# Performance work log

Hardware: AMD Instinct MI355X
Metric: run time of the kernel (lower is better)

The kernel has to match this reference:

```python
import jax, jax.numpy as jnp
import numpy as np


def setup_inputs() -> dict:
    key = jax.random.key(0)
    ks = jax.random.split(key, 5)
    B, DEC, ENC, H = 4, 256, 256, 512  # feature_dim = hl_size = 512, mlp hidden = 512
    decoder_states = jax.random.normal(ks[0], (B, DEC, H), dtype=jnp.float32)
    encoder_states = jax.random.normal(ks[1], (B, ENC, H), dtype=jnp.float32)
    ext_mask = jnp.zeros((B, DEC, ENC), dtype=bool)  # self.mask set externally; all-False here
    W_mlp = jax.random.normal(ks[2], (2 * H, H), dtype=jnp.float32) * 0.02  # Linear(2H -> H)
    b_mlp = jnp.zeros((H,), dtype=jnp.float32)
    W_out = jax.random.normal(ks[3], (H, 1), dtype=jnp.float32) * 0.02  # Linear(H -> 1)
    b_out = jnp.zeros((1,), dtype=jnp.float32)
    return {"decoder_states": decoder_states, "encoder_states": encoder_states,
            "ext_mask": ext_mask, "W_mlp": W_mlp, "b_mlp": b_mlp,
            "W_out": W_out, "b_out": b_out}


def reference(decoder_states, encoder_states, ext_mask, W_mlp, b_mlp, W_out, b_out):
    # decoder_states: [B, dec, H]; encoder_states: [B, enc, H]
    H = encoder_states.shape[-1]
    # pad mask: positions where encoder feature-0 equals 0.0 -> [B, 1, enc]
    pad_mask = (encoder_states == 0.0)[:, :, :1]
    pad_mask = jnp.swapaxes(pad_mask, 1, 2)  # [B, 1, enc]
    # cat(enc, dec) @ W_mlp  ==  enc @ W_mlp[:H] + dec @ W_mlp[H:]  (avoids 2H concat)
    enc_proj = jnp.einsum('beh,hm->bem', encoder_states, W_mlp[:H])   # [B, enc, Hm]
    dec_proj = jnp.einsum('bdh,hm->bdm', decoder_states, W_mlp[H:])   # [B, dec, Hm]
    hidden = jnp.tanh(dec_proj[:, :, None, :] + enc_proj[:, None, :, :] + b_mlp)  # [B, dec, enc, Hm]
    attn = jnp.einsum('bdem,mo->bde', hidden, W_out) + b_out[0]       # [B, dec, enc]
    attn = jnp.where(ext_mask, -jnp.inf, attn)
    attn = jnp.where(pad_mask, -jnp.inf, attn)
    attn = jax.nn.softmax(attn, axis=-1)
    context = jnp.einsum('bde,beh->bdh', attn, encoder_states)        # [B, dec, H]
    return (context, attn)
```

## Files before the change

### kernel.cpp

```cpp
#include <hip/hip_runtime.h>
#include <math.h>

#define B 4
#define DEC 256
#define ENC 256
#define HDIM 512

#define TANH_SCALE 2.8853900817779268f
#define LOG2E 1.4426950408889634f

__device__ __forceinline__ float fast_exp2(float x) { return __builtin_amdgcn_exp2f(x); }
__device__ __forceinline__ float fast_rcp(float x)  { return __builtin_amdgcn_rcpf(x); }

typedef __attribute__((ext_vector_type(8))) short bf16x8;
typedef __attribute__((ext_vector_type(4))) short bf16x4;
typedef __attribute__((ext_vector_type(4))) float f32x4;

__device__ __forceinline__ unsigned short bf16_rne(float x) {
    unsigned u = __float_as_uint(x);
    return (unsigned short)((u + 0x7FFFu + ((u >> 16) & 1u)) >> 16);
}
__device__ __forceinline__ float bf16_to_f(unsigned short h) {
    return __uint_as_float((unsigned)h << 16);
}

#define W_OFS(m, k) ((((long)(m) >> 4) << 13) + (((long)(k) >> 3) << 7) + (((m) & 15) << 3) + ((k) & 7))

__global__ __launch_bounds__(256) void convert_kernel(
    const float* __restrict__ enc, const float* __restrict__ dec,
    const float* __restrict__ Wmlp,
    unsigned short* __restrict__ Xh_e, unsigned short* __restrict__ Xl_e,
    unsigned short* __restrict__ Xh_d, unsigned short* __restrict__ Xl_d,
    unsigned short* __restrict__ Wh_e, unsigned short* __restrict__ Wl_e,
    unsigned short* __restrict__ Wh_d, unsigned short* __restrict__ Wl_d)
{
    const int tid = threadIdx.x, z = blockIdx.z;
    if (z < 2) {
        const float* X = z ? dec : enc;
        unsigned short* H = z ? Xh_d : Xh_e;
        unsigned short* L = z ? Xl_d : Xl_e;
        const long i8 = ((long)blockIdx.x * 256 + tid) * 8;
        float4 v0 = *(const float4*)(X + i8);
        float4 v1 = *(const float4*)(X + i8 + 4);
        float xs[8] = {v0.x, v0.y, v0.z, v0.w, v1.x, v1.y, v1.z, v1.w};
        bf16x8 hv, lv;
#pragma unroll
        for (int j = 0; j < 8; ++j) {
            unsigned short h = bf16_rne(xs[j]);
            hv[j] = (short)h;
            lv[j] = (short)bf16_rne(xs[j] - bf16_to_f(h));
        }
        *(bf16x8*)(H + i8) = hv;
        *(bf16x8*)(L + i8) = lv;
    } else {
        const float* Wsrc = Wmlp + (z == 3 ? (long)HDIM * HDIM : 0);
        unsigned short* H = (z == 3) ? Wh_d : Wh_e;
        unsigned short* L = (z == 3) ? Wl_d : Wl_e;
        const int t = blockIdx.x * 256 + tid;
        const int m = t & 511;
        const int k0 = (t >> 9) << 2;
        bf16x4 hv, lv;
#pragma unroll
        for (int j = 0; j < 4; ++j) {
            float x = Wsrc[(long)(k0 + j) * 512 + m];
            unsigned short h = bf16_rne(x);
            hv[j] = (short)h;
            lv[j] = (short)bf16_rne(x - bf16_to_f(h));
        }
        const long ofs = W_OFS(m, k0);
        *(bf16x4*)(H + ofs) = hv;
        *(bf16x4*)(L + ofs) = lv;
    }
}

__global__ __launch_bounds__(256) void proj_mfma_kernel(
    const unsigned short* __restrict__ Xh_e, const unsigned short* __restrict__ Xl_e,
    const unsigned short* __restrict__ Xh_d, const unsigned short* __restrict__ Xl_d,
    const unsigned short* __restrict__ Wh_e, const unsigned short* __restrict__ Wl_e,
    const unsigned short* __restrict__ Wh_d, const unsigned short* __restrict__ Wl_d,
    const float* __restrict__ bmlp,
    float* __restrict__ ET, float* __restrict__ Dmat)
{
    const int tid = threadIdx.x;
    const int wave = tid >> 6, lane = tid & 63;
    const int z = blockIdx.z;
    const int r0w = blockIdx.x * 64 + wave * 16;
    const int m0 = blockIdx.y * 32;
    const unsigned short* Xh = z ? Xh_d : Xh_e;
    const unsigned short* Xl = z ? Xl_d : Xl_e;
    const unsigned short* Wh = z ? Wh_d : Wh_e;
    const unsigned short* Wl = z ? Wl_d : Wl_e;

    const int col = lane & 15;
    const int quad = lane >> 4;

    const unsigned short* pah = Xh + (long)(r0w + col) * 512 + quad * 8;
    const unsigned short* pal = Xl + (long)(r0w + col) * 512 + quad * 8;
    const long bofs = ((long)(m0 >> 4) << 13) + (quad << 7) + (col << 3);
    const unsigned short* pb0h = Wh + bofs;
    const unsigned short* pb0l = Wl + bofs;
    const unsigned short* pb1h = Wh + bofs + 8192;
    const unsigned short* pb1l = Wl + bofs + 8192;

    f32x4 a0h = {0.f,0.f,0.f,0.f}, a0x = {0.f,0.f,0.f,0.f};
    f32x4 a1h = {0.f,0.f,0.f,0.f}, a1x = {0.f,0.f,0.f,0.f};

    bf16x8 Ah = *(const bf16x8*)pah,  Al = *(const bf16x8*)pal;
    bf16x8 B0h = *(const bf16x8*)pb0h, B0l = *(const bf16x8*)pb0l;
    bf16x8 B1h = *(const bf16x8*)pb1h, B1l = *(const bf16x8*)pb1l;

#pragma unroll 1
    for (int k0 = 0; k0 < 512; k0 += 32) {
        bf16x8 nAh = Ah, nAl = Al, nB0h = B0h, nB0l = B0l, nB1h = B1h, nB1l = B1l;
        if (k0 + 32 < 512) {
            nAh = *(const bf16x8*)(pah + k0 + 32);
            nAl = *(const bf16x8*)(pal + k0 + 32);
            const long ko = (long)(k0 + 32) << 4;
            nB0h = *(const bf16x8*)(pb0h + ko);
            nB0l = *(const bf16x8*)(pb0l + ko);
            nB1h = *(const bf16x8*)(pb1h + ko);
            nB1l = *(const bf16x8*)(pb1l + ko);
        }
        a0h = __builtin_amdgcn_mfma_f32_16x16x32_bf16(Ah, B0h, a0h, 0, 0, 0);
        a1h = __builtin_amdgcn_mfma_f32_16x16x32_bf16(Ah, B1h, a1h, 0, 0, 0);
        a0x = __builtin_amdgcn_mfma_f32_16x16x32_bf16(Ah, B0l, a0x, 0, 0, 0);
        a1x = __builtin_amdgcn_mfma_f32_16x16x32_bf16(Ah, B1l, a1x, 0, 0, 0);
        a0x = __builtin_amdgcn_mfma_f32_16x16x32_bf16(Al, B0h, a0x, 0, 0, 0);
        a1x = __builtin_amdgcn_mfma_f32_16x16x32_bf16(Al, B1h, a1x, 0, 0, 0);
        Ah = nAh; Al = nAl; B0h = nB0h; B0l = nB0l; B1h = nB1h; B1l = nB1l;
    }

    if (z == 0) {
        const int batch = r0w >> 8;
        const int e0 = (r0w & 255) + quad * 4;
        float* base = ET + (long)batch * HDIM * ENC;
        float4 v;
        v.x = fast_exp2((a0h[0] + a0x[0]) * TANH_SCALE);
        v.y = fast_exp2((a0h[1] + a0x[1]) * TANH_SCALE);
        v.z = fast_exp2((a0h[2] + a0x[2]) * TANH_SCALE);
        v.w = fast_exp2((a0h[3] + a0x[3]) * TANH_SCALE);
        *(float4*)&base[(long)(m0 + col) * ENC + e0] = v;
        v.x = fast_exp2((a1h[0] + a1x[0]) * TANH_SCALE);
        v.y = fast_exp2((a1h[1] + a1x[1]) * TANH_SCALE);
        v.z = fast_exp2((a1h[2] + a1x[2]) * TANH_SCALE);
        v.w = fast_exp2((a1h[3] + a1x[3]) * TANH_SCALE);
        *(float4*)&base[(long)(m0 + 16 + col) * ENC + e0] = v;
    } else {
        const float bq0 = bmlp[m0 + col];
        const float bq1 = bmlp[m0 + 16 + col];
        const int r = r0w + quad * 4;
#pragma unroll
        for (int i = 0; i < 4; ++i) {
            Dmat[(long)(r + i) * HDIM + m0 + col] =
                fast_exp2((a0h[i] + a0x[i] + bq0) * TANH_SCALE);
            Dmat[(long)(r + i) * HDIM + m0 + 16 + col] =
                fast_exp2((a1h[i] + a1x[i] + bq1) * TANH_SCALE);
        }
    }
}

__global__ __launch_bounds__(512) void attn_ctx_kernel(
    const float* __restrict__ Dmat, const float* __restrict__ ET,
    const float* __restrict__ wo,
    const float* __restrict__ enc, const unsigned char* __restrict__ extm,
    float* __restrict__ attn_out, float* __restrict__ ctx)
{
    __shared__ __align__(16) float ds[4][HDIM];
    __shared__ __align__(16) float wos[HDIM];
    __shared__ __align__(16) float p2[2][4][ENC];
    __shared__ __align__(16) float as4T[ENC][4];
    __shared__ float redm[4][4];
    __shared__ float reds[4][4];

    const int tid = threadIdx.x;
    const int b = blockIdx.z, d0 = blockIdx.x * 4;
    const long g0 = (long)b * DEC + d0;

    ((float4*)ds)[tid] = ((const float4*)(Dmat + g0 * HDIM))[tid];
    if (tid < 128) ((float4*)wos)[tid] = ((const float4*)wo)[tid];

    const int ty = tid >> 8;
    const int e = tid & 255;
    const float* ecol = ET + (long)b * HDIM * ENC + (long)(ty * 256) * ENC + e;

    float ev[16], nv[16];
#pragma unroll
    for (int j = 0; j < 16; ++j) ev[j] = ecol[j * ENC];
    __syncthreads();

    float acc[4] = {0.f, 0.f, 0.f, 0.f};
    for (int m = 0; m < 256; m += 16) {
        if (m + 16 < 256) {
#pragma unroll
            for (int j = 0; j < 16; ++j) nv[j] = ecol[(m + 16 + j) * ENC];
        }
        const int mb = ty * 256 + m;
        float4 dv[4][4], wv[4];
#pragma unroll
        for (int q = 0; q < 4; ++q) {
#pragma unroll
            for (int r = 0; r < 4; ++r)
                dv[r][q] = *(const float4*)&ds[r][mb + q * 4];
            wv[q] = *(const float4*)&wos[mb + q * 4];
        }
#pragma unroll
        for (int j = 0; j < 16; ++j) {
            float w = ((const float*)&wv[j >> 2])[j & 3];
#pragma unroll
            for (int r = 0; r < 4; ++r) {
                float t = fmaf(ev[j], ((const float*)&dv[r][j >> 2])[j & 3], 1.0f);
                acc[r] = fmaf(w, fast_rcp(t), acc[r]);
            }
        }
#pragma unroll
        for (int j = 0; j < 16; ++j) ev[j] = nv[j];
    }

#pragma unroll
    for (int r = 0; r < 4; ++r) p2[ty][r][e] = acc[r];
    __syncthreads();

    float l[4], p[4];
    const int wave = tid >> 6, lane = tid & 63;
    if (ty == 0) {
        const bool pad = (enc[((long)b * ENC + e) * HDIM] == 0.0f);
#pragma unroll
        for (int r = 0; r < 4; ++r) {
            float a = p2[0][r][e] + p2[1][r][e];
            bool xm = extm[(g0 + r) * ENC + e] != 0;
            l[r] = (pad || xm) ? -__builtin_inff() : -2.0f * a;
        }
        float mx[4] = {l[0], l[1], l[2], l[3]};
#pragma unroll
        for (int off = 32; off >= 1; off >>= 1) {
#pragma unroll
            for (int r = 0; r < 4; ++r)
                mx[r] = fmaxf(mx[r], __shfl_xor(mx[r], off, 64));
        }
        if (lane == 0) {
#pragma unroll
            for (int r = 0; r < 4; ++r) redm[wave][r] = mx[r];
        }
    }
    __syncthreads();
    if (ty == 0) {
        float s[4];
#pragma unroll
        for (int r = 0; r < 4; ++r) {
            float gm = fmaxf(fmaxf(redm[0][r], redm[1][r]),
                             fmaxf(redm[2][r], redm[3][r]));
            p[r] = fast_exp2((l[r] - gm) * LOG2E);
            s[r] = p[r];
        }
#pragma unroll
        for (int off = 32; off >= 1; off >>= 1) {
#pragma unroll
            for (int r = 0; r < 4; ++r)
                s[r] += __shfl_xor(s[r], off, 64);
        }
        if (lane == 0) {
#pragma unroll
            for (int r = 0; r < 4; ++r) reds[wave][r] = s[r];
        }
    }
    __syncthreads();
    if (ty == 0) {
        float4 pv;
        float pr[4];
#pragma unroll
        for (int r = 0; r < 4; ++r) {
            float gs = reds[0][r] + reds[1][r] + reds[2][r] + reds[3][r];
            pr[r] = p[r] * fast_rcp(gs);
            attn_out[(g0 + r) * ENC + e] = pr[r];
        }
        pv.x = pr[0]; pv.y = pr[1]; pv.z = pr[2]; pv.w = pr[3];
        *(float4*)&as4T[e][0] = pv;
    }
    __syncthreads();

    const int h = tid;
    const float* eh = enc + (long)b * ENC * HDIM + h;
    float ac0 = 0.f, ac1 = 0.f, ac2 = 0.f, ac3 = 0.f;
    float ebuf[8], nbuf[8];
#pragma unroll
    for (int j = 0; j < 8; ++j) ebuf[j] = eh[(long)j * HDIM];
    for (int e0 = 0; e0 < ENC; e0 += 8) {
        if (e0 + 8 < ENC) {
#pragma unroll
            for (int j = 0; j < 8; ++j) nbuf[j] = eh[(long)(e0 + 8 + j) * HDIM];
        }
#pragma unroll
        for (int j = 0; j < 8; ++j) {
            float4 prv = *(const float4*)&as4T[e0 + j][0];
            float ev4 = ebuf[j];
            ac0 = fmaf(prv.x, ev4, ac0);
            ac1 = fmaf(prv.y, ev4, ac1);
            ac2 = fmaf(prv.z, ev4, ac2);
            ac3 = fmaf(prv.w, ev4, ac3);
        }
#pragma unroll
        for (int j = 0; j < 8; ++j) ebuf[j] = nbuf[j];
    }
    ctx[(g0 + 0) * HDIM + h] = ac0;
    ctx[(g0 + 1) * HDIM + h] = ac1;
    ctx[(g0 + 2) * HDIM + h] = ac2;
    ctx[(g0 + 3) * HDIM + h] = ac3;
}

extern "C" void kernel_launch(void* const* d_in, const int* in_sizes, int n_in,
                              void* d_out, int out_size, void* d_ws, size_t ws_size,
                              hipStream_t stream) {
    const float* dec = (const float*)d_in[0];
    const float* enc = (const float*)d_in[1];
    const unsigned char* extm = (const unsigned char*)d_in[2];
    const float* Wmlp = (const float*)d_in[3];
    const float* bmlp = (const float*)d_in[4];
    const float* Wout = (const float*)d_in[5];

    float* ctx = (float*)d_out;
    float* attn = ctx + (size_t)B * DEC * HDIM;

    const size_t F = (size_t)B * DEC * HDIM;
    float* ET = (float*)d_ws;
    float* Dmat = ET + F;
    unsigned short* Xh_e = (unsigned short*)(Dmat + F);
    unsigned short* Xl_e = Xh_e + F;
    unsigned short* Xh_d = Xl_e + F;
    unsigned short* Xl_d = Xh_d + F;
    unsigned short* Wh_e = Xl_d + F;
    unsigned short* Wl_e = Wh_e + HDIM * HDIM;
    unsigned short* Wh_d = Wl_e + HDIM * HDIM;
    unsigned short* Wl_d = Wh_d + HDIM * HDIM;

    convert_kernel<<<dim3(256, 1, 4), 256, 0, stream>>>(
        enc, dec, Wmlp, Xh_e, Xl_e, Xh_d, Xl_d, Wh_e, Wl_e, Wh_d, Wl_d);
    proj_mfma_kernel<<<dim3(16, 16, 2), 256, 0, stream>>>(
        Xh_e, Xl_e, Xh_d, Xl_d, Wh_e, Wl_e, Wh_d, Wl_d, bmlp, ET, Dmat);
    attn_ctx_kernel<<<dim3(DEC / 4, 1, B), 512, 0, stream>>>(
        Dmat, ET, Wout, enc, extm, attn, ctx);
}
```

Measured before the change: 118.0 us.

## Retile attention score loop to 8 m-groups x 4 enc columns per thread

Each thread now covers 4 encoder columns (float4 loads) over a 64-wide slice of the hidden dim, in place of one column over 256 hidden values. The 8 partial sums are reduced through a larger shared buffer. The softmax stage is spread across all 512 threads, each handling 2 decoder rows, so half the block no longer sits idle. The aims are vectorized global loads, fewer LDS reads per reciprocal, and better thread use in the softmax. The cost is more shared memory for the partial sums and a longer reduction over 8 partials.

```diff
diff --git a/kernel.cpp b/kernel.cpp
--- a/kernel.cpp
+++ b/kernel.cpp
@@ -167,7 +167,7 @@
 {
     __shared__ __align__(16) float ds[4][HDIM];
     __shared__ __align__(16) float wos[HDIM];
-    __shared__ __align__(16) float p2[2][4][ENC];
+    __shared__ __align__(16) float p8[8][4][ENC];
     __shared__ __align__(16) float as4T[ENC][4];
     __shared__ float redm[4][4];
     __shared__ float reds[4][4];
@@ -179,102 +179,98 @@
     ((float4*)ds)[tid] = ((const float4*)(Dmat + g0 * HDIM))[tid];
     if (tid < 128) ((float4*)wos)[tid] = ((const float4*)wo)[tid];
 
+    const int mg = tid >> 6;
+    const int e4 = (tid & 63) * 4;
+    const int mbase = mg * 64;
+    const float* ep = ET + (long)b * HDIM * ENC + (long)mbase * ENC + e4;
+
+    float4 E0 = *(const float4*)(ep);
+    float4 E1 = *(const float4*)(ep + ENC);
+    __syncthreads();
+
+    float acc[4][4] = {};
+    for (int i = 0; i < 64; i += 2) {
+        float4 Ea = E0, Eb = E1;
+        if (i + 2 < 64) {
+            E0 = *(const float4*)(ep + (long)(i + 2) * ENC);
+            E1 = *(const float4*)(ep + (long)(i + 3) * ENC);
+        }
+        const int m = mbase + i;
+        const float w0 = wos[m], w1 = wos[m + 1];
+#pragma unroll
+        for (int r = 0; r < 4; ++r) {
+            const float dr0 = ds[r][m];
+            const float dr1 = ds[r][m + 1];
+#pragma unroll
+            for (int j = 0; j < 4; ++j) {
+                float ea = ((const float*)&Ea)[j];
+                float eb = ((const float*)&Eb)[j];
+                acc[r][j] = fmaf(w0, fast_rcp(fmaf(ea, dr0, 1.0f)), acc[r][j]);
+                acc[r][j] = fmaf(w1, fast_rcp(fmaf(eb, dr1, 1.0f)), acc[r][j]);
+            }
+        }
+    }
+#pragma unroll
+    for (int r = 0; r < 4; ++r) {
+        float4 v = make_float4(acc[r][0], acc[r][1], acc[r][2], acc[r][3]);
+        *(float4*)&p8[mg][r][e4] = v;
+    }
+    __syncthreads();
+
     const int ty = tid >> 8;
     const int e = tid & 255;
-    const float* ecol = ET + (long)b * HDIM * ENC + (long)(ty * 256) * ENC + e;
-
-    float ev[16], nv[16];
-#pragma unroll
-    for (int j = 0; j < 16; ++j) ev[j] = ecol[j * ENC];
-    __syncthreads();
-
-    float acc[4] = {0.f, 0.f, 0.f, 0.f};
-    for (int m = 0; m < 256; m += 16) {
-        if (m + 16 < 256) {
-#pragma unroll
-            for (int j = 0; j < 16; ++j) nv[j] = ecol[(m + 16 + j) * ENC];
-        }
-        const int mb = ty * 256 + m;
-        float4 dv[4][4], wv[4];
-#pragma unroll
-        for (int q = 0; q < 4; ++q) {
-#pragma unroll
-            for (int r = 0; r < 4; ++r)
-                dv[r][q] = *(const float4*)&ds[r][mb + q * 4];
-            wv[q] = *(const float4*)&wos[mb + q * 4];
-        }
-#pragma unroll
-        for (int j = 0; j < 16; ++j) {
-            float w = ((const float*)&wv[j >> 2])[j & 3];
-#pragma unroll
-            for (int r = 0; r < 4; ++r) {
-                float t = fmaf(ev[j], ((const float*)&dv[r][j >> 2])[j & 3], 1.0f);
-                acc[r] = fmaf(w, fast_rcp(t), acc[r]);
-            }
-        }
-#pragma unroll
-        for (int j = 0; j < 16; ++j) ev[j] = nv[j];
-    }
-
-#pragma unroll
-    for (int r = 0; r < 4; ++r) p2[ty][r][e] = acc[r];
-    __syncthreads();
-
-    float l[4], p[4];
     const int wave = tid >> 6, lane = tid & 63;
-    if (ty == 0) {
-        const bool pad = (enc[((long)b * ENC + e) * HDIM] == 0.0f);
-#pragma unroll
-        for (int r = 0; r < 4; ++r) {
-            float a = p2[0][r][e] + p2[1][r][e];
-            bool xm = extm[(g0 + r) * ENC + e] != 0;
-            l[r] = (pad || xm) ? -__builtin_inff() : -2.0f * a;
-        }
-        float mx[4] = {l[0], l[1], l[2], l[3]};
-#pragma unroll
-        for (int off = 32; off >= 1; off >>= 1) {
-#pragma unroll
-            for (int r = 0; r < 4; ++r)
-                mx[r] = fmaxf(mx[r], __shfl_xor(mx[r], off, 64));
-        }
-        if (lane == 0) {
-#pragma unroll
-            for (int r = 0; r < 4; ++r) redm[wave][r] = mx[r];
-        }
-    }
-    __syncthreads();
-    if (ty == 0) {
-        float s[4];
-#pragma unroll
-        for (int r = 0; r < 4; ++r) {
-            float gm = fmaxf(fmaxf(redm[0][r], redm[1][r]),
-                             fmaxf(redm[2][r], redm[3][r]));
-            p[r] = fast_exp2((l[r] - gm) * LOG2E);
-            s[r] = p[r];
-        }
-#pragma unroll
-        for (int off = 32; off >= 1; off >>= 1) {
-#pragma unroll
-            for (int r = 0; r < 4; ++r)
-                s[r] += __shfl_xor(s[r], off, 64);
-        }
-        if (lane == 0) {
-#pragma unroll
-            for (int r = 0; r < 4; ++r) reds[wave][r] = s[r];
-        }
-    }
-    __syncthreads();
-    if (ty == 0) {
-        float4 pv;
-        float pr[4];
-#pragma unroll
-        for (int r = 0; r < 4; ++r) {
-            float gs = reds[0][r] + reds[1][r] + reds[2][r] + reds[3][r];
-            pr[r] = p[r] * fast_rcp(gs);
-            attn_out[(g0 + r) * ENC + e] = pr[r];
-        }
-        pv.x = pr[0]; pv.y = pr[1]; pv.z = pr[2]; pv.w = pr[3];
-        *(float4*)&as4T[e][0] = pv;
+
+    const bool pad = (enc[((long)b * ENC + e) * HDIM] == 0.0f);
+    float l[2], p[2];
+#pragma unroll
+    for (int rl = 0; rl < 2; ++rl) {
+        const int r = ty * 2 + rl;
+        float a = 0.f;
+#pragma unroll
+        for (int q = 0; q < 8; ++q) a += p8[q][r][e];
+        const bool xm = extm[(g0 + r) * ENC + e] != 0;
+        l[rl] = (pad || xm) ? -__builtin_inff() : -2.0f * a;
+    }
+    float mx[2] = {l[0], l[1]};
+#pragma unroll
+    for (int off = 32; off >= 1; off >>= 1) {
+#pragma unroll
+        for (int rl = 0; rl < 2; ++rl)
+            mx[rl] = fmaxf(mx[rl], __shfl_xor(mx[rl], off, 64));
+    }
+    if (lane == 0) {
+        redm[ty * 2 + 0][wave & 3] = mx[0];
+        redm[ty * 2 + 1][wave & 3] = mx[1];
+    }
+    __syncthreads();
+    float s[2];
+#pragma unroll
+    for (int rl = 0; rl < 2; ++rl) {
+        const int r = ty * 2 + rl;
+        const float gm = fmaxf(fmaxf(redm[r][0], redm[r][1]),
+                               fmaxf(redm[r][2], redm[r][3]));
+        p[rl] = fast_exp2((l[rl] - gm) * LOG2E);
+        s[rl] = p[rl];
+    }
+#pragma unroll
+    for (int off = 32; off >= 1; off >>= 1) {
+#pragma unroll
+        for (int rl = 0; rl < 2; ++rl)
+            s[rl] += __shfl_xor(s[rl], off, 64);
+    }
+    if (lane == 0) {
+        reds[ty * 2 + 0][wave & 3] = s[0];
+        reds[ty * 2 + 1][wave & 3] = s[1];
+    }
+    __syncthreads();
+#pragma unroll
+    for (int rl = 0; rl < 2; ++rl) {
+        const int r = ty * 2 + rl;
+        const float gs = reds[r][0] + reds[r][1] + reds[r][2] + reds[r][3];
+        const float pr = p[rl] * fast_rcp(gs);
+        attn_out[(g0 + r) * ENC + e] = pr;
+        as4T[e][r] = pr;
     }
     __syncthreads();
 
```

New measurement: 116.1 us. Within noise of the previous version (-1.6%).
